# Kernel tuning notes

Hardware: AMD Instinct MI355X
Metric: run time of the kernel (lower is better)

The kernel has to match this reference:

```python
import jax, jax.numpy as jnp
import numpy as np

N = 50000   # n_nodes
E = 500000  # n_edges
D = 128     # input_dim == hidden_dim
L = 2       # n_layers
K = 5       # Chebyshev filter size


def setup_inputs() -> dict:
    key = jax.random.key(0)
    k0, k1, k2, k3, k4 = jax.random.split(key, 5)
    scale = 1.0 / np.sqrt(D)
    return {
        "edge_index": jax.random.randint(k0, (2, E), 0, N),
        "edge_weight": jax.random.uniform(k1, (E,), dtype=jnp.float32),
        "emb": jax.random.uniform(k2, (N, D), dtype=jnp.float32, minval=-1.0, maxval=1.0),
        "Wx": jax.random.normal(k3, (L, 3, K, D, D), dtype=jnp.float32) * scale,
        "bx": jnp.zeros((L, 3, D), dtype=jnp.float32),
        "Wh": jax.random.normal(k4, (L, 3, K, D, D), dtype=jnp.float32) * scale,
        "bh": jnp.zeros((L, 3, D), dtype=jnp.float32),
    }


def reference(edge_index, edge_weight, emb, Wx, bx, Wh, bh):
    src, dst = edge_index[0], edge_index[1]
    # ChebConv sym-normalized scaled Laplacian with lambda_max=2:
    # L_hat = L - I = -D^{-1/2} A D^{-1/2} (zero diagonal)
    deg = jax.ops.segment_sum(edge_weight, src, num_segments=N)
    dinv = jnp.where(deg > 0, deg ** -0.5, 0.0)
    w = -dinv[src] * edge_weight * dinv[dst]  # [E]

    def prop(x):  # L_hat @ x via gather/scatter over edges
        return jax.ops.segment_sum(w[:, None] * x[src], dst, num_segments=N)

    def cheb(x, W, b):  # sum_k T_k(L_hat) x W_k + b
        Tx0 = x
        out = Tx0 @ W[0]
        Tx1 = prop(Tx0)
        out = out + Tx1 @ W[1]
        for k in range(2, K):
            Tx2 = 2.0 * prop(Tx1) - Tx0
            out = out + Tx2 @ W[k]
            Tx0, Tx1 = Tx1, Tx2
        return out + b

    x = emb
    hidden_states = []
    for l in range(L):
        H = jnp.ones((N, D), x.dtype)  # init__hidd: ones
        Z = jax.nn.sigmoid(cheb(x, Wx[l, 0], bx[l, 0]) + cheb(H, Wh[l, 0], bh[l, 0]))
        R = jax.nn.sigmoid(cheb(x, Wx[l, 1], bx[l, 1]) + cheb(H, Wh[l, 1], bh[l, 1]))
        Ht = jnp.tanh(cheb(x, Wx[l, 2], bx[l, 2]) + cheb(H * R, Wh[l, 2], bh[l, 2]))
        Hn = Z * H + (1.0 - Z) * Ht
        h = jax.nn.relu(Hn)  # dropout is identity in eval mode
        hidden_states.append(h)
        x = h
    return x  # == hidden_states[-1]
```

## Files before the change

kernel.cpp:

```cpp
#include <hip/hip_runtime.h>
#include <math.h>

#define NN 50000
#define EE 500000
#define DD 128
#define KK 5
#define LL 2

#define PSZ32 ((size_t)NN * 32)

typedef _Float16 f16x8 __attribute__((ext_vector_type(8)));
typedef float f32x4 __attribute__((ext_vector_type(4)));

__device__ __forceinline__ ushort f2h(float x) {
    union { _Float16 h; ushort u; } v; v.h = (_Float16)x; return v.u;
}


__global__ __launch_bounds__(256) void edge_pass1(
    const int* __restrict__ src, const int* __restrict__ dst,
    const float* __restrict__ ew,
    float* __restrict__ deg, int* __restrict__ hist)
{
    int e = blockIdx.x * blockDim.x + threadIdx.x;
    if (e >= EE) return;
    atomicAdd(&deg[src[e]], ew[e]);
    atomicAdd(&hist[dst[e]], 1);
}

__global__ __launch_bounds__(256) void dinv_kernel(
    const float* __restrict__ deg, float* __restrict__ dinv)
{
    int i = blockIdx.x * blockDim.x + threadIdx.x;
    if (i >= NN) return;
    float d = deg[i];
    dinv[i] = (d > 0.f) ? (1.f / sqrtf(d)) : 0.f;
}

#define SCAN_C ((NN + 1023) / 1024)
__global__ __launch_bounds__(1024) void scan_kernel(
    const int* __restrict__ hist, int* __restrict__ row_ptr)
{
    __shared__ int sums[1024];
    const int t = threadIdx.x;
    const int base = t * SCAN_C;
    int local[SCAN_C];
    int s = 0;
#pragma unroll
    for (int j = 0; j < SCAN_C; ++j) {
        int i = base + j;
        int v = (i < NN) ? hist[i] : 0;
        s += v;
        local[j] = s;
    }
    sums[t] = s;
    __syncthreads();
    for (int off = 1; off < 1024; off <<= 1) {
        int v = (t >= off) ? sums[t - off] : 0;
        __syncthreads();
        sums[t] += v;
        __syncthreads();
    }
    int excl = sums[t] - s;
    if (t == 0) row_ptr[0] = 0;
#pragma unroll
    for (int j = 0; j < SCAN_C; ++j) {
        int i = base + j;
        if (i < NN) row_ptr[i + 1] = excl + local[j];
    }
}

__global__ __launch_bounds__(256) void copy_fill(
    const int* __restrict__ row_ptr, int* __restrict__ fill)
{
    int i = blockIdx.x * blockDim.x + threadIdx.x;
    if (i < NN) fill[i] = row_ptr[i];
}

__global__ __launch_bounds__(256) void edge_scatter(
    const int* __restrict__ src, const int* __restrict__ dst,
    const float* __restrict__ ew, const float* __restrict__ dinv,
    int* __restrict__ fill,
    int* __restrict__ src_srt, float* __restrict__ w_srt)
{
    int e = blockIdx.x * blockDim.x + threadIdx.x;
    if (e >= EE) return;
    int s = src[e], t = dst[e];
    float w = -dinv[s] * ew[e] * dinv[t];
    int pos = atomicAdd(&fill[t], 1);
    src_srt[pos] = s;
    w_srt[pos] = w;
}

__global__ __launch_bounds__(256) void propv_kernel(
    const int* __restrict__ rp, const int* __restrict__ ss, const float* __restrict__ sw,
    const float* __restrict__ tin, const float* __restrict__ tprev, float* __restrict__ tout,
    float alpha, float beta, int ones_in, int ones_prev)
{
    int i = blockIdx.x * blockDim.x + threadIdx.x;
    if (i >= NN) return;
    float acc = 0.f;
    int e0 = rp[i], e1 = rp[i + 1];
    int e = e0;
    for (; e + 4 <= e1; e += 4) {
        float t0 = ones_in ? 1.f : tin[ss[e]];
        float t1v = ones_in ? 1.f : tin[ss[e + 1]];
        float t2v = ones_in ? 1.f : tin[ss[e + 2]];
        float t3v = ones_in ? 1.f : tin[ss[e + 3]];
        acc += sw[e] * t0 + sw[e + 1] * t1v + sw[e + 2] * t2v + sw[e + 3] * t3v;
    }
    for (; e < e1; ++e) {
        float tv = ones_in ? 1.f : tin[ss[e]];
        acc += sw[e] * tv;
    }
    float pv = ones_prev ? 1.f : (tprev ? tprev[i] : 0.f);
    tout[i] = alpha * acc + beta * pv;
}

__global__ __launch_bounds__(128) void colsum_kernel(
    const float* __restrict__ Wh, float* __restrict__ scol)
{
    int b = blockIdx.x;
    int k = b % KK;
    int g = (b / KK) % 2;
    int l = b / (2 * KK);
    int d = threadIdx.x;
    const float* Wp = Wh + ((size_t)((l * 3 + g) * KK + k)) * DD * DD;
    float s = 0.f;
    for (int r = 0; r < DD; ++r) s += Wp[r * DD + d];
    scol[((size_t)((l * 2 + g) * KK + k)) * DD + d] = s;
}

__global__ __launch_bounds__(256) void wconv_f16(
    const float* __restrict__ W, ushort* __restrict__ out, int mode)
{
    int t = blockIdx.x;
    int st = (mode == 0) ? t : ((t / KK) * 3 + 2) * KK + (t % KK);
    const float* Wp = W + (size_t)st * DD * DD;
    ushort* op = out + (size_t)t * DD * DD;
    for (int idx = threadIdx.x; idx < DD * DD; idx += 256) {
        int rb = idx >> 7, c = idx & 127;
        float w = Wp[c * DD + rb];
        int byte = rb * 256 + (((c * 2) ^ ((rb & 7) << 4)));
        *(ushort*)((char*)op + byte) = f2h(w);
    }
}

__global__ __launch_bounds__(256) void f32_to_f16_panel(
    const float* __restrict__ in, ushort* __restrict__ out, int n8)
{
    int j = blockIdx.x * blockDim.x + threadIdx.x;
    if (j >= n8) return;
    int flat = j * 8;
    int i = flat >> 7;
    int d0 = flat & 127;
    float4 a = *(const float4*)(in + (size_t)i * DD + d0);
    float4 b = *(const float4*)(in + (size_t)i * DD + d0 + 4);
    f16x8 o;
    o[0] = (_Float16)a.x; o[1] = (_Float16)a.y; o[2] = (_Float16)a.z; o[3] = (_Float16)a.w;
    o[4] = (_Float16)b.x; o[5] = (_Float16)b.y; o[6] = (_Float16)b.z; o[7] = (_Float16)b.w;
    *(f16x8*)(out + (size_t)(d0 >> 5) * PSZ32 + (size_t)i * 32 + (d0 & 31)) = o;
}

__global__ __launch_bounds__(256) void prop_mat(
    const int* __restrict__ rp, const int* __restrict__ ss, const float* __restrict__ sw,
    const ushort* __restrict__ x, const ushort* __restrict__ prev,
    ushort* __restrict__ out, float alpha, float beta)
{
    const int p = blockIdx.x & 3;
    const int node = (blockIdx.x >> 2) * 64 + (threadIdx.x >> 2);
    if (node >= NN) return;
    const int lane8 = (threadIdx.x & 3) * 8;
    const ushort* xp = x + (size_t)p * PSZ32 + lane8;
    float acc[8];
#pragma unroll
    for (int j = 0; j < 8; ++j) acc[j] = 0.f;
    int e0 = rp[node], e1 = rp[node + 1];
    int e = e0;
    for (; e + 8 <= e1; e += 8) {
        int s0 = ss[e], s1 = ss[e + 1], s2 = ss[e + 2], s3 = ss[e + 3];
        int s4 = ss[e + 4], s5 = ss[e + 5], s6 = ss[e + 6], s7 = ss[e + 7];
        float w0 = sw[e], w1 = sw[e + 1], w2 = sw[e + 2], w3 = sw[e + 3];
        float w4 = sw[e + 4], w5 = sw[e + 5], w6 = sw[e + 6], w7 = sw[e + 7];
        f16x8 r0 = *(const f16x8*)(xp + (size_t)s0 * 32);
        f16x8 r1 = *(const f16x8*)(xp + (size_t)s1 * 32);
        f16x8 r2 = *(const f16x8*)(xp + (size_t)s2 * 32);
        f16x8 r3 = *(const f16x8*)(xp + (size_t)s3 * 32);
        f16x8 r4 = *(const f16x8*)(xp + (size_t)s4 * 32);
        f16x8 r5 = *(const f16x8*)(xp + (size_t)s5 * 32);
        f16x8 r6 = *(const f16x8*)(xp + (size_t)s6 * 32);
        f16x8 r7 = *(const f16x8*)(xp + (size_t)s7 * 32);
#pragma unroll
        for (int j = 0; j < 8; ++j)
            acc[j] += w0 * (float)r0[j] + w1 * (float)r1[j] + w2 * (float)r2[j] + w3 * (float)r3[j]
                    + w4 * (float)r4[j] + w5 * (float)r5[j] + w6 * (float)r6[j] + w7 * (float)r7[j];
    }
    for (; e + 4 <= e1; e += 4) {
        int s0 = ss[e], s1 = ss[e + 1], s2 = ss[e + 2], s3 = ss[e + 3];
        float w0 = sw[e], w1 = sw[e + 1], w2 = sw[e + 2], w3 = sw[e + 3];
        f16x8 r0 = *(const f16x8*)(xp + (size_t)s0 * 32);
        f16x8 r1 = *(const f16x8*)(xp + (size_t)s1 * 32);
        f16x8 r2 = *(const f16x8*)(xp + (size_t)s2 * 32);
        f16x8 r3 = *(const f16x8*)(xp + (size_t)s3 * 32);
#pragma unroll
        for (int j = 0; j < 8; ++j)
            acc[j] += w0 * (float)r0[j] + w1 * (float)r1[j] + w2 * (float)r2[j] + w3 * (float)r3[j];
    }
    for (; e < e1; ++e) {
        int s = ss[e];
        float w = sw[e];
        f16x8 r = *(const f16x8*)(xp + (size_t)s * 32);
#pragma unroll
        for (int j = 0; j < 8; ++j) acc[j] += w * (float)r[j];
    }
    f16x8 o;
    if (beta != 0.f && prev) {
        f16x8 pv = *(const f16x8*)(prev + (size_t)p * PSZ32 + (size_t)node * 32 + lane8);
#pragma unroll
        for (int j = 0; j < 8; ++j) o[j] = (_Float16)(alpha * acc[j] + beta * (float)pv[j]);
    } else {
#pragma unroll
        for (int j = 0; j < 8; ++j) o[j] = (_Float16)(alpha * acc[j]);
    }
    *(f16x8*)(out + (size_t)p * PSZ32 + (size_t)node * 32 + lane8) = o;
}

template<int NFR>
__device__ __forceinline__ void mm_gate(
    const ushort* __restrict__ const* Ts, const ushort* __restrict__ Wg,
    ushort* Bs, const int* rowg, const bool* ok,
    int tid, int lk, int lr, f32x4 acc[NFR][8])
{
#pragma unroll
    for (int fr = 0; fr < NFR; ++fr)
#pragma unroll
        for (int fc = 0; fc < 8; ++fc) acc[fr][fc] = (f32x4){0.f, 0.f, 0.f, 0.f};
#pragma unroll
    for (int k = 0; k < KK; ++k) {
        const ushort* Bg = Wg + (size_t)k * (DD * DD);
        __syncthreads();
#pragma unroll
        for (int i = 0; i < 8; ++i) {
            int off = i * 4096 + tid * 16;
            uint4 v = *(const uint4*)((const char*)Bg + off);
            *(uint4*)((char*)Bs + off) = v;
        }
        f16x8 a[NFR][4];
#pragma unroll
        for (int fr = 0; fr < NFR; ++fr) {
#pragma unroll
            for (int ko = 0; ko < 4; ++ko) {
                const ushort* ap = Ts[k] + (size_t)ko * PSZ32
                                 + (size_t)rowg[fr] * 32 + lk * 8;
                if (ok[fr]) a[fr][ko] = *(const f16x8*)ap;
                else a[fr][ko] = (f16x8){0, 0, 0, 0, 0, 0, 0, 0};
            }
        }
        __syncthreads();
#pragma unroll
        for (int ko = 0; ko < 4; ++ko) {
            const int cb = ko * 64 + lk * 16;
#pragma unroll
            for (int fc = 0; fc < 8; ++fc) {
                int rb = fc * 16 + lr;
                int byte = (rb * 256 + cb) ^ ((rb & 7) << 4);
                f16x8 bfrag = *(const f16x8*)((const char*)Bs + byte);
#pragma unroll
                for (int fr = 0; fr < NFR; ++fr)
                    acc[fr][fc] = __builtin_amdgcn_mfma_f32_16x16x32_f16(a[fr][ko], bfrag, acc[fr][fc], 0, 0, 0);
            }
        }
    }
}

__device__ __forceinline__ int xcd_swz(int b, int nwg) {
    int xcd = b & 7, idx = b >> 3;
    int q = nwg >> 3, rr = nwg & 7;
    int start = (xcd < rr) ? xcd * (q + 1) : rr * (q + 1) + (xcd - rr) * q;
    return start + idx;
}

__global__ __launch_bounds__(256) void cheb_mm_mfma(
    const ushort* __restrict__ T0, const ushort* __restrict__ T1,
    const ushort* __restrict__ T2, const ushort* __restrict__ T3,
    const ushort* __restrict__ T4,
    const ushort* __restrict__ Wt, int gate_stride,
    float* __restrict__ outbase, size_t out_stride, int ngates)
{
    __shared__ ushort Bs[DD * DD];
    const int lin = xcd_swz(blockIdx.x, gridDim.x);
    const int tile = lin / ngates;
    const int g = lin - tile * ngates;

    const int tid = threadIdx.x;
    const int lane = tid & 63;
    const int wid = tid >> 6;
    const int lr = lane & 15;
    const int lk = lane >> 4;
    const int r0 = tile * 128;
    const ushort* Ts[5] = {T0, T1, T2, T3, T4};

    int rowg[2] = {r0 + wid * 32 + lr, r0 + wid * 32 + lr + 16};
    bool ok[2] = {rowg[0] < NN, rowg[1] < NN};

    f32x4 acc[2][8];
    mm_gate<2>(Ts, Wt + (size_t)g * gate_stride, Bs, rowg, ok, tid, lk, lr, acc);

    float* outp = outbase + (size_t)g * out_stride;
#pragma unroll
    for (int fr = 0; fr < 2; ++fr) {
#pragma unroll
        for (int j = 0; j < 4; ++j) {
            int grow = r0 + wid * 32 + fr * 16 + lk * 4 + j;
            if (grow < NN) {
#pragma unroll
                for (int fc = 0; fc < 8; ++fc) {
                    int col = fc * 16 + lr;
                    outp[(size_t)grow * DD + col] = acc[fr][fc][j];
                }
            }
        }
    }
}

__global__ __launch_bounds__(256) void cheb_mm_final(
    const ushort* __restrict__ T0, const ushort* __restrict__ T1,
    const ushort* __restrict__ T2, const ushort* __restrict__ T3,
    const ushort* __restrict__ T4,
    const ushort* __restrict__ Wt,
    const float* __restrict__ Xh, const float* __restrict__ Xz,
    const float* __restrict__ bx, const float* __restrict__ bh, int l,
    float* __restrict__ out, ushort* __restrict__ h16, int write_f32)
{
    __shared__ ushort Bs[DD * DD];
    const int tile = xcd_swz(blockIdx.x, gridDim.x);
    const int tid = threadIdx.x;
    const int lane = tid & 63;
    const int wid = tid >> 6;
    const int lr = lane & 15;
    const int lk = lane >> 4;
    const int r0 = tile * 64;
    const ushort* Ts[5] = {T0, T1, T2, T3, T4};

    int rowg[1] = {r0 + wid * 16 + lr};
    bool ok[1] = {rowg[0] < NN};

    f32x4 acc[1][8];
    mm_gate<1>(Ts, Wt, Bs, rowg, ok, tid, lk, lr, acc);

    const float* b0 = bx + (size_t)(l * 3 + 2) * DD;
    const float* b1 = bh + (size_t)(l * 3 + 2) * DD;
#pragma unroll
    for (int j = 0; j < 4; ++j) {
        int grow = r0 + wid * 16 + lk * 4 + j;
        if (grow < NN) {
#pragma unroll
            for (int fc = 0; fc < 8; ++fc) {
                int d = fc * 16 + lr;
                size_t idx = (size_t)grow * DD + d;
                float pre = acc[0][fc][j] + Xh[idx] + b0[d] + b1[d];
                float ht = tanhf(pre);
                float z = Xz[idx];
                float hn = z + (1.f - z) * ht;
                float h = hn > 0.f ? hn : 0.f;
                if (write_f32) out[idx] = h;
                else h16[(size_t)(d >> 5) * PSZ32 + (size_t)grow * 32 + (d & 31)] = f2h(h);
            }
        }
    }
}

__global__ __launch_bounds__(256) void gate_zr_kernel(
    float* __restrict__ Xz, const float* __restrict__ Xr, ushort* __restrict__ Xr_f16,
    const float* __restrict__ tvec, const float* __restrict__ scol,
    const float* __restrict__ bx, const float* __restrict__ bh, int l)
{
    int idx = blockIdx.x * blockDim.x + threadIdx.x;
    if (idx >= NN * DD) return;
    int i = idx >> 7;
    int d = idx & 127;
    float t1 = tvec[i], t2 = tvec[NN + i], t3 = tvec[2 * NN + i], t4 = tvec[3 * NN + i];

    const float* s0 = scol + (size_t)((l * 2 + 0) * KK) * DD;
    float hz = s0[d] + t1 * s0[DD + d] + t2 * s0[2 * DD + d] + t3 * s0[3 * DD + d] + t4 * s0[4 * DD + d];
    float z = Xz[idx] + bx[(l * 3 + 0) * DD + d] + bh[(l * 3 + 0) * DD + d] + hz;
    Xz[idx] = 1.f / (1.f + expf(-z));

    const float* s1 = scol + (size_t)((l * 2 + 1) * KK) * DD;
    float hr = s1[d] + t1 * s1[DD + d] + t2 * s1[2 * DD + d] + t3 * s1[3 * DD + d] + t4 * s1[4 * DD + d];
    float r = Xr[idx] + bx[(l * 3 + 1) * DD + d] + bh[(l * 3 + 1) * DD + d] + hr;
    Xr_f16[(size_t)(d >> 5) * PSZ32 + (size_t)i * 32 + (d & 31)] = f2h(1.f / (1.f + expf(-r)));
}


extern "C" void kernel_launch(void* const* d_in, const int* in_sizes, int n_in,
                              void* d_out, int out_size, void* d_ws, size_t ws_size,
                              hipStream_t stream)
{
    const int*   ei  = (const int*)d_in[0];
    const float* ew  = (const float*)d_in[1];
    const float* emb = (const float*)d_in[2];
    const float* Wx  = (const float*)d_in[3];
    const float* bx  = (const float*)d_in[4];
    const float* Wh  = (const float*)d_in[5];
    const float* bh  = (const float*)d_in[6];
    float* out = (float*)d_out;

    const int* src = ei;
    const int* dst = ei + EE;

    char* ws = (char*)d_ws;
    size_t off = 0;
    auto alloc = [&](size_t nbytes) -> char* {
        char* p = ws + off;
        off = (off + nbytes + 255) & ~(size_t)255;
        return p;
    };
    float*  deg     = (float*)alloc((size_t)NN * 4);
    float*  dinv    = (float*)alloc((size_t)NN * 4);
    int*    hist    = (int*)alloc((size_t)(NN + 1) * 4);
    int*    row_ptr = (int*)alloc((size_t)(NN + 1) * 4);
    int*    fill    = (int*)alloc((size_t)(NN + 1) * 4);
    int*    src_srt = (int*)alloc((size_t)EE * 4);
    float*  w_srt   = (float*)alloc((size_t)EE * 4);
    float*  tvec    = (float*)alloc((size_t)4 * NN * 4);
    float*  scol    = (float*)alloc((size_t)LL * 2 * KK * DD * 4);
    float*  X       = (float*)alloc((size_t)3 * NN * DD * 4);
    ushort* Th      = (ushort*)alloc((size_t)4 * NN * DD * 2);
    ushort* x_f16   = (ushort*)alloc((size_t)NN * DD * 2);
    ushort* Xr_f16  = (ushort*)alloc((size_t)NN * DD * 2);
    ushort* WxT     = (ushort*)alloc((size_t)LL * 3 * KK * DD * DD * 2);
    ushort* WhT2    = (ushort*)alloc((size_t)LL * KK * DD * DD * 2);
    (void)ws_size; (void)in_sizes; (void)n_in; (void)out_size;

    float* Xz = X;
    float* Xr = X + (size_t)NN * DD;
    float* Xh = X + (size_t)2 * NN * DD;
    ushort* T1 = Th;
    ushort* T2 = Th + (size_t)NN * DD;
    ushort* T3 = Th + (size_t)2 * NN * DD;
    ushort* T4 = Th + (size_t)3 * NN * DD;

    const int EG = (EE + 255) / 256;
    const int NG = (NN + 255) / 256;
    const int PG = ((NN + 63) / 64) * 4;
    const int ELG = (NN * DD + 255) / 256;
    const int MMG = (NN + 127) / 128;
    const int MMG2 = (NN + 63) / 64;
    const int CVG = (NN * DD / 8 + 255) / 256;
    const int GATE_STRIDE = KK * DD * DD;

    hipMemsetAsync(deg, 0, (size_t)NN * 4, stream);
    hipMemsetAsync(hist, 0, (size_t)(NN + 1) * 4, stream);

    edge_pass1<<<EG, 256, 0, stream>>>(src, dst, ew, deg, hist);
    dinv_kernel<<<NG, 256, 0, stream>>>(deg, dinv);
    scan_kernel<<<1, 1024, 0, stream>>>(hist, row_ptr);
    copy_fill<<<NG, 256, 0, stream>>>(row_ptr, fill);
    edge_scatter<<<EG, 256, 0, stream>>>(src, dst, ew, dinv, fill, src_srt, w_srt);

    float* t1 = tvec;
    float* t2 = tvec + NN;
    float* t3 = tvec + 2 * NN;
    float* t4 = tvec + 3 * NN;
    propv_kernel<<<NG, 256, 0, stream>>>(row_ptr, src_srt, w_srt, nullptr, nullptr, t1, 1.f,  0.f, 1, 0);
    propv_kernel<<<NG, 256, 0, stream>>>(row_ptr, src_srt, w_srt, t1, nullptr,      t2, 2.f, -1.f, 0, 1);
    propv_kernel<<<NG, 256, 0, stream>>>(row_ptr, src_srt, w_srt, t2, t1,           t3, 2.f, -1.f, 0, 0);
    propv_kernel<<<NG, 256, 0, stream>>>(row_ptr, src_srt, w_srt, t3, t2,           t4, 2.f, -1.f, 0, 0);

    colsum_kernel<<<LL * 2 * KK, 128, 0, stream>>>(Wh, scol);

    wconv_f16<<<LL * 3 * KK, 256, 0, stream>>>(Wx, WxT, 0);
    wconv_f16<<<LL * KK, 256, 0, stream>>>(Wh, WhT2, 1);

    f32_to_f16_panel<<<CVG, 256, 0, stream>>>(emb, x_f16, NN * DD / 8);

    for (int l = 0; l < LL; ++l) {
        prop_mat<<<PG, 256, 0, stream>>>(row_ptr, src_srt, w_srt, x_f16, nullptr, T1, 1.f,  0.f);
        prop_mat<<<PG, 256, 0, stream>>>(row_ptr, src_srt, w_srt, T1,    x_f16,   T2, 2.f, -1.f);
        prop_mat<<<PG, 256, 0, stream>>>(row_ptr, src_srt, w_srt, T2,    T1,      T3, 2.f, -1.f);
        prop_mat<<<PG, 256, 0, stream>>>(row_ptr, src_srt, w_srt, T3,    T2,      T4, 2.f, -1.f);

        cheb_mm_mfma<<<MMG * 3, 256, 0, stream>>>(x_f16, T1, T2, T3, T4,
                                             WxT + (size_t)l * 3 * GATE_STRIDE, GATE_STRIDE,
                                             Xz, (size_t)NN * DD, 3);

        gate_zr_kernel<<<ELG, 256, 0, stream>>>(Xz, Xr, Xr_f16, tvec, scol, bx, bh, l);

        prop_mat<<<PG, 256, 0, stream>>>(row_ptr, src_srt, w_srt, Xr_f16, nullptr, T1, 1.f,  0.f);
        prop_mat<<<PG, 256, 0, stream>>>(row_ptr, src_srt, w_srt, T1,     Xr_f16,  T2, 2.f, -1.f);
        prop_mat<<<PG, 256, 0, stream>>>(row_ptr, src_srt, w_srt, T2,     T1,      T3, 2.f, -1.f);
        prop_mat<<<PG, 256, 0, stream>>>(row_ptr, src_srt, w_srt, T3,     T2,      T4, 2.f, -1.f);

        cheb_mm_final<<<MMG2, 256, 0, stream>>>(Xr_f16, T1, T2, T3, T4,
                                               WhT2 + (size_t)l * GATE_STRIDE,
                                               Xh, Xz, bx, bh, l,
                                               out, x_f16, (l == LL - 1) ? 1 : 0);
    }
}
```

Before: 862.8 us.

## Pre-swizzle weights into MFMA fragment order and drop LDS staging

The weight conversion kernel now writes each 128x128 f16 weight matrix in the exact per-lane MFMA B-fragment order, so the Chebyshev matmul kernels read B fragments straight from global memory (L2-resident) instead of staging them through shared memory with barriers. This removes the LDS copy and two __syncthreads per K step and frees 32KB of LDS per block, at the cost of repeated global/L2 reads of weights by every wave. Separately, the sparse propagation kernel uses nontemporal loads for the CSR indices and weights and a nontemporal store for its output, to reduce cache pollution.

```diff
diff --git a/kernel.cpp b/kernel.cpp
--- a/kernel.cpp
+++ b/kernel.cpp
@@ -11,6 +11,7 @@
 
 typedef _Float16 f16x8 __attribute__((ext_vector_type(8)));
 typedef float f32x4 __attribute__((ext_vector_type(4)));
+typedef unsigned int u32x4 __attribute__((ext_vector_type(4)));
 
 __device__ __forceinline__ ushort f2h(float x) {
     union { _Float16 h; ushort u; } v; v.h = (_Float16)x; return v.u;
@@ -131,7 +132,7 @@
     scol[((size_t)((l * 2 + g) * KK + k)) * DD + d] = s;
 }
 
-__global__ __launch_bounds__(256) void wconv_f16(
+__global__ __launch_bounds__(256) void wconv_frag(
     const float* __restrict__ W, ushort* __restrict__ out, int mode)
 {
     int t = blockIdx.x;
@@ -139,10 +140,14 @@
     const float* Wp = W + (size_t)st * DD * DD;
     ushort* op = out + (size_t)t * DD * DD;
     for (int idx = threadIdx.x; idx < DD * DD; idx += 256) {
-        int rb = idx >> 7, c = idx & 127;
-        float w = Wp[c * DD + rb];
-        int byte = rb * 256 + (((c * 2) ^ ((rb & 7) << 4)));
-        *(ushort*)((char*)op + byte) = f2h(w);
+        int j  = idx & 7;
+        int lk = (idx >> 3) & 3;
+        int lr = (idx >> 5) & 15;
+        int fc = (idx >> 9) & 7;
+        int ko = idx >> 12;
+        int dout = fc * 16 + lr;
+        int din  = ko * 32 + lk * 8 + j;
+        op[idx] = f2h(Wp[din * DD + dout]);
     }
 }
 
@@ -178,10 +183,22 @@
     int e0 = rp[node], e1 = rp[node + 1];
     int e = e0;
     for (; e + 8 <= e1; e += 8) {
-        int s0 = ss[e], s1 = ss[e + 1], s2 = ss[e + 2], s3 = ss[e + 3];
-        int s4 = ss[e + 4], s5 = ss[e + 5], s6 = ss[e + 6], s7 = ss[e + 7];
-        float w0 = sw[e], w1 = sw[e + 1], w2 = sw[e + 2], w3 = sw[e + 3];
-        float w4 = sw[e + 4], w5 = sw[e + 5], w6 = sw[e + 6], w7 = sw[e + 7];
+        int s0 = __builtin_nontemporal_load(ss + e);
+        int s1 = __builtin_nontemporal_load(ss + e + 1);
+        int s2 = __builtin_nontemporal_load(ss + e + 2);
+        int s3 = __builtin_nontemporal_load(ss + e + 3);
+        int s4 = __builtin_nontemporal_load(ss + e + 4);
+        int s5 = __builtin_nontemporal_load(ss + e + 5);
+        int s6 = __builtin_nontemporal_load(ss + e + 6);
+        int s7 = __builtin_nontemporal_load(ss + e + 7);
+        float w0 = __builtin_nontemporal_load(sw + e);
+        float w1 = __builtin_nontemporal_load(sw + e + 1);
+        float w2 = __builtin_nontemporal_load(sw + e + 2);
+        float w3 = __builtin_nontemporal_load(sw + e + 3);
+        float w4 = __builtin_nontemporal_load(sw + e + 4);
+        float w5 = __builtin_nontemporal_load(sw + e + 5);
+        float w6 = __builtin_nontemporal_load(sw + e + 6);
+        float w7 = __builtin_nontemporal_load(sw + e + 7);
         f16x8 r0 = *(const f16x8*)(xp + (size_t)s0 * 32);
         f16x8 r1 = *(const f16x8*)(xp + (size_t)s1 * 32);
         f16x8 r2 = *(const f16x8*)(xp + (size_t)s2 * 32);
@@ -213,23 +230,22 @@
 #pragma unroll
         for (int j = 0; j < 8; ++j) acc[j] += w * (float)r[j];
     }
-    f16x8 o;
+    union { f16x8 v; u32x4 u; } o;
     if (beta != 0.f && prev) {
         f16x8 pv = *(const f16x8*)(prev + (size_t)p * PSZ32 + (size_t)node * 32 + lane8);
 #pragma unroll
-        for (int j = 0; j < 8; ++j) o[j] = (_Float16)(alpha * acc[j] + beta * (float)pv[j]);
+        for (int j = 0; j < 8; ++j) o.v[j] = (_Float16)(alpha * acc[j] + beta * (float)pv[j]);
     } else {
 #pragma unroll
-        for (int j = 0; j < 8; ++j) o[j] = (_Float16)(alpha * acc[j]);
-    }
-    *(f16x8*)(out + (size_t)p * PSZ32 + (size_t)node * 32 + lane8) = o;
+        for (int j = 0; j < 8; ++j) o.v[j] = (_Float16)(alpha * acc[j]);
+    }
+    __builtin_nontemporal_store(o.u, (u32x4*)(out + (size_t)p * PSZ32 + (size_t)node * 32 + lane8));
 }
 
 template<int NFR>
 __device__ __forceinline__ void mm_gate(
     const ushort* __restrict__ const* Ts, const ushort* __restrict__ Wg,
-    ushort* Bs, const int* rowg, const bool* ok,
-    int tid, int lk, int lr, f32x4 acc[NFR][8])
+    const int* rowg, const bool* ok, int lk, int lr, f32x4 acc[NFR][8])
 {
 #pragma unroll
     for (int fr = 0; fr < NFR; ++fr)
@@ -237,14 +253,6 @@
         for (int fc = 0; fc < 8; ++fc) acc[fr][fc] = (f32x4){0.f, 0.f, 0.f, 0.f};
 #pragma unroll
     for (int k = 0; k < KK; ++k) {
-        const ushort* Bg = Wg + (size_t)k * (DD * DD);
-        __syncthreads();
-#pragma unroll
-        for (int i = 0; i < 8; ++i) {
-            int off = i * 4096 + tid * 16;
-            uint4 v = *(const uint4*)((const char*)Bg + off);
-            *(uint4*)((char*)Bs + off) = v;
-        }
         f16x8 a[NFR][4];
 #pragma unroll
         for (int fr = 0; fr < NFR; ++fr) {
@@ -256,18 +264,16 @@
                 else a[fr][ko] = (f16x8){0, 0, 0, 0, 0, 0, 0, 0};
             }
         }
-        __syncthreads();
+        const char* WB = (const char*)(Wg + (size_t)k * DD * DD);
+        const int lo = lr * 64 + lk * 16;
 #pragma unroll
         for (int ko = 0; ko < 4; ++ko) {
-            const int cb = ko * 64 + lk * 16;
 #pragma unroll
             for (int fc = 0; fc < 8; ++fc) {
-                int rb = fc * 16 + lr;
-                int byte = (rb * 256 + cb) ^ ((rb & 7) << 4);
-                f16x8 bfrag = *(const f16x8*)((const char*)Bs + byte);
+                f16x8 b = *(const f16x8*)(WB + ((ko * 8 + fc) << 10) + lo);
 #pragma unroll
                 for (int fr = 0; fr < NFR; ++fr)
-                    acc[fr][fc] = __builtin_amdgcn_mfma_f32_16x16x32_f16(a[fr][ko], bfrag, acc[fr][fc], 0, 0, 0);
+                    acc[fr][fc] = __builtin_amdgcn_mfma_f32_16x16x32_f16(a[fr][ko], b, acc[fr][fc], 0, 0, 0);
             }
         }
     }
@@ -287,14 +293,12 @@
     const ushort* __restrict__ Wt, int gate_stride,
     float* __restrict__ outbase, size_t out_stride, int ngates)
 {
-    __shared__ ushort Bs[DD * DD];
     const int lin = xcd_swz(blockIdx.x, gridDim.x);
     const int tile = lin / ngates;
     const int g = lin - tile * ngates;
 
-    const int tid = threadIdx.x;
-    const int lane = tid & 63;
-    const int wid = tid >> 6;
+    const int lane = threadIdx.x & 63;
+    const int wid = threadIdx.x >> 6;
     const int lr = lane & 15;
     const int lk = lane >> 4;
     const int r0 = tile * 128;
@@ -304,7 +308,7 @@
     bool ok[2] = {rowg[0] < NN, rowg[1] < NN};
 
     f32x4 acc[2][8];
-    mm_gate<2>(Ts, Wt + (size_t)g * gate_stride, Bs, rowg, ok, tid, lk, lr, acc);
+    mm_gate<2>(Ts, Wt + (size_t)g * gate_stride, rowg, ok, lk, lr, acc);
 
     float* outp = outbase + (size_t)g * out_stride;
 #pragma unroll
@@ -332,11 +336,9 @@
     const float* __restrict__ bx, const float* __restrict__ bh, int l,
     float* __restrict__ out, ushort* __restrict__ h16, int write_f32)
 {
-    __shared__ ushort Bs[DD * DD];
     const int tile = xcd_swz(blockIdx.x, gridDim.x);
-    const int tid = threadIdx.x;
-    const int lane = tid & 63;
-    const int wid = tid >> 6;
+    const int lane = threadIdx.x & 63;
+    const int wid = threadIdx.x >> 6;
     const int lr = lane & 15;
     const int lk = lane >> 4;
     const int r0 = tile * 64;
@@ -346,7 +348,7 @@
     bool ok[1] = {rowg[0] < NN};
 
     f32x4 acc[1][8];
-    mm_gate<1>(Ts, Wt, Bs, rowg, ok, tid, lk, lr, acc);
+    mm_gate<1>(Ts, Wt, rowg, ok, lk, lr, acc);
 
     const float* b0 = bx + (size_t)(l * 3 + 2) * DD;
     const float* b1 = bh + (size_t)(l * 3 + 2) * DD;
@@ -470,8 +472,8 @@
 
     colsum_kernel<<<LL * 2 * KK, 128, 0, stream>>>(Wh, scol);
 
-    wconv_f16<<<LL * 3 * KK, 256, 0, stream>>>(Wx, WxT, 0);
-    wconv_f16<<<LL * KK, 256, 0, stream>>>(Wh, WhT2, 1);
+    wconv_frag<<<LL * 3 * KK, 256, 0, stream>>>(Wx, WxT, 0);
+    wconv_frag<<<LL * KK, 256, 0, stream>>>(Wh, WhT2, 1);
 
     f32_to_f16_panel<<<CVG, 256, 0, stream>>>(emb, x_f16, NN * DD / 8);
 
```

Result: slower. 1.084 ms (+25.6%).

## Stage two Chebyshev weight tiles per sync round and fold fill init into scan

Applied to the files above, without the earlier changes.

The MFMA Chebyshev matmul now loads two 128x128 weight tiles into a doubled shared buffer per round, so five K tiles take three sync rounds instead of five. This halves the barrier count but doubles LDS use to 64KB per block, which may cut occupancy. Separately, the scan kernel now writes the fill offsets directly, which removes the copy_fill launch. The u32x4 typedef is added but unused.

```diff
diff --git a/kernel.cpp b/kernel.cpp
--- a/kernel.cpp
+++ b/kernel.cpp
@@ -11,6 +11,7 @@
 
 typedef _Float16 f16x8 __attribute__((ext_vector_type(8)));
 typedef float f32x4 __attribute__((ext_vector_type(4)));
+typedef unsigned int u32x4 __attribute__((ext_vector_type(4)));
 
 __device__ __forceinline__ ushort f2h(float x) {
     union { _Float16 h; ushort u; } v; v.h = (_Float16)x; return v.u;
@@ -39,7 +40,7 @@
 
 #define SCAN_C ((NN + 1023) / 1024)
 __global__ __launch_bounds__(1024) void scan_kernel(
-    const int* __restrict__ hist, int* __restrict__ row_ptr)
+    const int* __restrict__ hist, int* __restrict__ row_ptr, int* __restrict__ fill)
 {
     __shared__ int sums[1024];
     const int t = threadIdx.x;
@@ -66,15 +67,11 @@
 #pragma unroll
     for (int j = 0; j < SCAN_C; ++j) {
         int i = base + j;
-        if (i < NN) row_ptr[i + 1] = excl + local[j];
-    }
-}
-
-__global__ __launch_bounds__(256) void copy_fill(
-    const int* __restrict__ row_ptr, int* __restrict__ fill)
-{
-    int i = blockIdx.x * blockDim.x + threadIdx.x;
-    if (i < NN) fill[i] = row_ptr[i];
+        if (i < NN) {
+            row_ptr[i + 1] = excl + local[j];
+            fill[i] = excl + (j ? local[j - 1] : 0);
+        }
+    }
 }
 
 __global__ __launch_bounds__(256) void edge_scatter(
@@ -236,38 +233,52 @@
 #pragma unroll
         for (int fc = 0; fc < 8; ++fc) acc[fr][fc] = (f32x4){0.f, 0.f, 0.f, 0.f};
 #pragma unroll
-    for (int k = 0; k < KK; ++k) {
-        const ushort* Bg = Wg + (size_t)k * (DD * DD);
+    for (int rnd = 0; rnd < 3; ++rnd) {
+        const int kb = rnd * 2;
+        const int ntile = (rnd == 2) ? 1 : 2;
         __syncthreads();
 #pragma unroll
-        for (int i = 0; i < 8; ++i) {
-            int off = i * 4096 + tid * 16;
-            uint4 v = *(const uint4*)((const char*)Bg + off);
-            *(uint4*)((char*)Bs + off) = v;
-        }
-        f16x8 a[NFR][4];
-#pragma unroll
-        for (int fr = 0; fr < NFR; ++fr) {
-#pragma unroll
-            for (int ko = 0; ko < 4; ++ko) {
-                const ushort* ap = Ts[k] + (size_t)ko * PSZ32
-                                 + (size_t)rowg[fr] * 32 + lk * 8;
-                if (ok[fr]) a[fr][ko] = *(const f16x8*)ap;
-                else a[fr][ko] = (f16x8){0, 0, 0, 0, 0, 0, 0, 0};
+        for (int t = 0; t < 2; ++t) {
+            if (t < ntile) {
+                const ushort* Bg = Wg + (size_t)(kb + t) * (DD * DD);
+#pragma unroll
+                for (int i = 0; i < 8; ++i) {
+                    int off = i * 4096 + tid * 16;
+                    uint4 v = *(const uint4*)((const char*)Bg + off);
+                    *(uint4*)((char*)Bs + t * 32768 + off) = v;
+                }
             }
         }
         __syncthreads();
 #pragma unroll
-        for (int ko = 0; ko < 4; ++ko) {
-            const int cb = ko * 64 + lk * 16;
-#pragma unroll
-            for (int fc = 0; fc < 8; ++fc) {
-                int rb = fc * 16 + lr;
-                int byte = (rb * 256 + cb) ^ ((rb & 7) << 4);
-                f16x8 bfrag = *(const f16x8*)((const char*)Bs + byte);
-#pragma unroll
-                for (int fr = 0; fr < NFR; ++fr)
-                    acc[fr][fc] = __builtin_amdgcn_mfma_f32_16x16x32_f16(a[fr][ko], bfrag, acc[fr][fc], 0, 0, 0);
+        for (int t = 0; t < 2; ++t) {
+            if (t < ntile) {
+                const int k = kb + t;
+                f16x8 a[NFR][4];
+#pragma unroll
+                for (int fr = 0; fr < NFR; ++fr) {
+#pragma unroll
+                    for (int ko = 0; ko < 4; ++ko) {
+                        const ushort* ap = Ts[k] + (size_t)ko * PSZ32
+                                         + (size_t)rowg[fr] * 32 + lk * 8;
+                        if (ok[fr]) a[fr][ko] = *(const f16x8*)ap;
+                        else a[fr][ko] = (f16x8){0, 0, 0, 0, 0, 0, 0, 0};
+                    }
+                }
+                const char* base = (const char*)Bs + t * 32768;
+#pragma unroll
+                for (int ko = 0; ko < 4; ++ko) {
+                    const int cb = ko * 64 + lk * 16;
+#pragma unroll
+                    for (int fc = 0; fc < 8; ++fc) {
+                        int rb = fc * 16 + lr;
+                        int byte = (rb * 256 + cb) ^ ((rb & 7) << 4);
+                        f16x8 bfrag = *(const f16x8*)(base + byte);
+#pragma unroll
+                        for (int fr = 0; fr < NFR; ++fr)
+                            acc[fr][fc] = __builtin_amdgcn_mfma_f32_16x16x32_f16(a[fr][ko], bfrag, acc[fr][fc], 0, 0, 0);
+                    }
+                }
             }
         }
     }
@@ -287,7 +298,7 @@
     const ushort* __restrict__ Wt, int gate_stride,
     float* __restrict__ outbase, size_t out_stride, int ngates)
 {
-    __shared__ ushort Bs[DD * DD];
+    __shared__ ushort Bs[DD * DD * 2];
     const int lin = xcd_swz(blockIdx.x, gridDim.x);
     const int tile = lin / ngates;
     const int g = lin - tile * ngates;
@@ -332,7 +343,7 @@
     const float* __restrict__ bx, const float* __restrict__ bh, int l,
     float* __restrict__ out, ushort* __restrict__ h16, int write_f32)
 {
-    __shared__ ushort Bs[DD * DD];
+    __shared__ ushort Bs[DD * DD * 2];
     const int tile = xcd_swz(blockIdx.x, gridDim.x);
     const int tid = threadIdx.x;
     const int lane = tid & 63;
@@ -455,8 +466,7 @@
 
     edge_pass1<<<EG, 256, 0, stream>>>(src, dst, ew, deg, hist);
     dinv_kernel<<<NG, 256, 0, stream>>>(deg, dinv);
-    scan_kernel<<<1, 1024, 0, stream>>>(hist, row_ptr);
-    copy_fill<<<NG, 256, 0, stream>>>(row_ptr, fill);
+    scan_kernel<<<1, 1024, 0, stream>>>(hist, row_ptr, fill);
     edge_scatter<<<EG, 256, 0, stream>>>(src, dst, ew, dinv, fill, src_srt, w_srt);
 
     float* t1 = tvec;
```

Result: slower. 884.2 us (+2.5%).
